# Performance work log

Measured on AMD Instinct MI355X. Metric: run time of the kernel, lower is better.

The kernel has to match this reference:

```python
import jax, jax.numpy as jnp
import numpy as np

EPS = 1e-5  # torch BatchNorm default eps


def _bn(x, g, b, axes):
    # Training-mode batch norm (biased variance, as torch uses for normalization)
    m = x.mean(axes, keepdims=True)
    v = x.var(axes, keepdims=True)
    sh = [1] * x.ndim
    sh[1] = x.shape[1]
    return (x - m) / jnp.sqrt(v + EPS) * g.reshape(sh) + b.reshape(sh)


def _conv2d(x, w, b, pad):
    y = jax.lax.conv_general_dilated(x, w, (1, 1), ((pad, pad), (pad, pad)),
                                     dimension_numbers=('NCHW', 'OIHW', 'NCHW'))
    return y + b.reshape(1, -1, 1, 1)


def _conv3d(x, w, b):
    # kernel (1,1,3), padding (0,0,1)
    y = jax.lax.conv_general_dilated(x, w, (1, 1, 1), ((0, 0), (0, 0), (1, 1)),
                                     dimension_numbers=('NCDHW', 'OIDHW', 'NCDHW'))
    return y + b.reshape(1, -1, 1, 1, 1)


def _block(x, w, b, g, be):
    return jax.nn.relu(_bn(_conv2d(x, w, b, 1), g, be, (0, 2, 3)))


def _pool(x):
    return jax.lax.reduce_window(x, -jnp.inf, jax.lax.max, (1, 1, 2, 2), (1, 1, 2, 2), 'VALID')


def _interp_axis(x, axis):
    # bilinear, align_corners=True, scale factor 2 along one axis
    n = x.shape[axis]
    out = 2 * n
    pos = jnp.linspace(0.0, n - 1.0, out)
    lo = jnp.floor(pos).astype(jnp.int32)
    hi = jnp.minimum(lo + 1, n - 1)
    w = (pos - lo).astype(x.dtype)
    sh = [1] * x.ndim
    sh[axis] = out
    w = w.reshape(sh)
    return jnp.take(x, lo, axis=axis) * (1 - w) + jnp.take(x, hi, axis=axis) * w


def _upsample(x):
    return _interp_axis(_interp_axis(x, 2), 3)


def _forward(x, tp_w1, tp_b1, tp_g1, tp_be1, tp_w2, tp_b2, tp_g2, tp_be2,
             range_w, doppler_w,
             enc1_w, enc1_b, enc1_g, enc1_be,
             enc2_w, enc2_b, enc2_g, enc2_be,
             enc3_w, enc3_b, enc3_g, enc3_be,
             dec3_w, dec3_b, dec3_g, dec3_be,
             dec2_w, dec2_b, dec2_g, dec2_be,
             dec1_w, dec1_b, dec1_g, dec1_be,
             out_w, out_b):
    # x: [B, RX, C, S, 2] -> [B, 2, RX, C, S]
    h = jnp.transpose(x, (0, 4, 1, 2, 3))
    h = jax.nn.relu(_bn(_conv3d(h, tp_w1, tp_b1), tp_g1, tp_be1, (0, 2, 3, 4)))
    h = jax.nn.relu(_bn(_conv3d(h, tp_w2, tp_b2), tp_g2, tp_be2, (0, 2, 3, 4)))
    h = jnp.transpose(h, (0, 2, 3, 4, 1)).sum(axis=1)  # sum over RX -> [B, C, S, 2]
    xr, xi = h[..., 0], h[..., 1]
    # Range DFT (quadruple loop in torch == two complex matmuls)
    Wr, Wi = range_w[..., 0], range_w[..., 1]  # [S, R]
    rr = jnp.einsum('bcs,sr->bcr', xr, Wr) - jnp.einsum('bcs,sr->bcr', xi, Wi)
    ri = jnp.einsum('bcs,sr->bcr', xr, Wi) + jnp.einsum('bcs,sr->bcr', xi, Wr)
    # Doppler DFT over chirps
    Dr, Di = doppler_w[..., 0], doppler_w[..., 1]  # [C, D]
    rdr = jnp.einsum('bcr,cd->bdr', rr, Dr) - jnp.einsum('bcr,cd->bdr', ri, Di)
    rdi = jnp.einsum('bcr,cd->bdr', rr, Di) + jnp.einsum('bcr,cd->bdr', ri, Dr)
    rd = jnp.stack([rdr, rdi], axis=1)  # [B, 2, D, R]
    # RadarNet U-Net
    e1 = _block(rd, enc1_w, enc1_b, enc1_g, enc1_be)
    p1 = _pool(e1)
    e2 = _block(p1, enc2_w, enc2_b, enc2_g, enc2_be)
    p2 = _pool(e2)
    e3 = _block(p2, enc3_w, enc3_b, enc3_g, enc3_be)
    d3 = _block(e3, dec3_w, dec3_b, dec3_g, dec3_be)
    u2 = _upsample(d3) + e2
    d2 = _block(u2, dec2_w, dec2_b, dec2_g, dec2_be)
    u1 = _upsample(d2) + e1
    d1 = _block(u1, dec1_w, dec1_b, dec1_g, dec1_be)
    out = jax.nn.sigmoid(_conv2d(d1, out_w, out_b, 0))
    return jnp.transpose(out, (0, 2, 3, 1))  # [B, D, R, 1]


def setup_inputs() -> dict:
    key = jax.random.key(0)
    ctr = [0]

    def rn(shape, scale=1.0):
        ctr[0] += 1
        return jax.random.normal(jax.random.fold_in(key, ctr[0]), shape, dtype=jnp.float32) * scale

    B, RX, C, S, D, R = 16, 4, 128, 256, 128, 256
    inp = {
        'x': rn((B, RX, C, S, 2)),
        'tp_w1': rn((8, 2, 1, 1, 3), 0.4), 'tp_b1': jnp.zeros(8), 'tp_g1': jnp.ones(8), 'tp_be1': jnp.zeros(8),
        'tp_w2': rn((2, 8, 1, 1, 3), 0.2), 'tp_b2': jnp.zeros(2), 'tp_g2': jnp.ones(2), 'tp_be2': jnp.zeros(2),
        'range_w': rn((S, R, 2)), 'doppler_w': rn((C, D, 2)),
        'enc1_w': rn((32, 2, 3, 3), 0.1), 'enc1_b': jnp.zeros(32), 'enc1_g': jnp.ones(32), 'enc1_be': jnp.zeros(32),
        'enc2_w': rn((64, 32, 3, 3), 0.05), 'enc2_b': jnp.zeros(64), 'enc2_g': jnp.ones(64), 'enc2_be': jnp.zeros(64),
        'enc3_w': rn((128, 64, 3, 3), 0.04), 'enc3_b': jnp.zeros(128), 'enc3_g': jnp.ones(128), 'enc3_be': jnp.zeros(128),
        'dec3_w': rn((64, 128, 3, 3), 0.03), 'dec3_b': jnp.zeros(64), 'dec3_g': jnp.ones(64), 'dec3_be': jnp.zeros(64),
        'dec2_w': rn((32, 64, 3, 3), 0.04), 'dec2_b': jnp.zeros(32), 'dec2_g': jnp.ones(32), 'dec2_be': jnp.zeros(32),
        'dec1_w': rn((16, 32, 3, 3), 0.05), 'dec1_b': jnp.zeros(16), 'dec1_g': jnp.ones(16), 'dec1_be': jnp.zeros(16),
        'out_w': rn((1, 16, 1, 1), 0.25), 'out_b': jnp.zeros(1),
    }
    return inp


def reference(x, tp_w1, tp_b1, tp_g1, tp_be1, tp_w2, tp_b2, tp_g2, tp_be2,
              range_w, doppler_w,
              enc1_w, enc1_b, enc1_g, enc1_be,
              enc2_w, enc2_b, enc2_g, enc2_be,
              enc3_w, enc3_b, enc3_g, enc3_be,
              dec3_w, dec3_b, dec3_g, dec3_be,
              dec2_w, dec2_b, dec2_g, dec2_be,
              dec1_w, dec1_b, dec1_g, dec1_be,
              out_w, out_b):
    return _forward(x, tp_w1, tp_b1, tp_g1, tp_be1, tp_w2, tp_b2, tp_g2, tp_be2,
                    range_w, doppler_w,
                    enc1_w, enc1_b, enc1_g, enc1_be,
                    enc2_w, enc2_b, enc2_g, enc2_be,
                    enc3_w, enc3_b, enc3_g, enc3_be,
                    dec3_w, dec3_b, dec3_g, dec3_be,
                    dec2_w, dec2_b, dec2_g, dec2_be,
                    dec1_w, dec1_b, dec1_g, dec1_be,
                    out_w, out_b)
```

## Files before the change

kernel.cpp:

```cpp
#include <hip/hip_runtime.h>
#include <cmath>

constexpr int Bn = 16, RXn = 4, Cn = 128, Sn = 256, Dn = 128, Rn = 256;

typedef __attribute__((ext_vector_type(8))) short bf16x8;
typedef __attribute__((ext_vector_type(4))) float f32x4;
typedef unsigned short u16;
typedef unsigned int u32;
typedef __attribute__((ext_vector_type(4))) u16 u16x4;
typedef __attribute__((ext_vector_type(8))) u16 u16x8;
typedef __attribute__((ext_vector_type(2))) u32 u32x2;
typedef __attribute__((ext_vector_type(4))) u32 u32x4;

__device__ __forceinline__ u16 f2bf(float f) {
  union { float f; u32 u; } v; v.f = f;
  const u32 r = v.u + 0x7FFFu + ((v.u >> 16) & 1u);
  return (u16)(r >> 16);
}
__device__ __forceinline__ float bf2f(u16 h) {
  union { u32 u; float f; } v; v.u = (u32)h << 16; return v.f;
}
__device__ __forceinline__ u32 cvtpk(float lo, float hi) {
  u32 r;
  asm("v_cvt_pk_bf16_f32 %0, %1, %2" : "=v"(r) : "v"(lo), "v"(hi));
  return r;
}
__device__ __forceinline__ void split2(float a, float b, u32& hi, u32& lo) {
  hi = cvtpk(a, b);
  union { u32 u; float f; } va, vb;
  va.u = hi << 16;
  vb.u = hi & 0xFFFF0000u;
  lo = cvtpk(a - va.f, b - vb.f);
}
__device__ __forceinline__ void ld8bf(const u16* __restrict__ p, float* v) {
  const u16x8 h = *(const u16x8*)p;
#pragma unroll
  for (int k = 0; k < 8; ++k) v[k] = bf2f(h[k]);
}

__device__ __forceinline__ void pack_seg(const float* __restrict__ w, u16* __restrict__ wpk,
                                         int CIN, int COUT, int gid, int gsz) {
  const int total = COUT * CIN * 9;
  const int chunks = CIN >> 5;
  for (int idx = gid; idx < total; idx += gsz) {
    const int j = idx & 7;
    const int l = (idx >> 3) & 63;
    const int rest = idx >> 9;
    const int t = rest % 9;
    const int rest2 = rest / 9;
    const int q = rest2 % chunks;
    const int mf = rest2 / chunks;
    const int co = mf * 16 + (l & 15);
    const int ci = q * 32 + ((l >> 4) << 3) + j;
    wpk[idx] = f2bf(w[((size_t)co * CIN + ci) * 9 + t]);
  }
}

__global__ __launch_bounds__(256) void k_pack_stats(
    const float* __restrict__ e2w, const float* __restrict__ e3w,
    const float* __restrict__ d3w, const float* __restrict__ d2w,
    const float* __restrict__ d1w,
    const float* __restrict__ range_w, const float* __restrict__ dopp_w,
    u16* __restrict__ p_e2, u16* __restrict__ p_e3,
    u16* __restrict__ p_d3, u16* __restrict__ p_d2,
    u16* __restrict__ p_d1,
    u16* __restrict__ A1h, u16* __restrict__ A1l,
    u16* __restrict__ A2h, u16* __restrict__ A2l,
    const float* __restrict__ x, const float* __restrict__ w1,
    float* __restrict__ part) {
  if (blockIdx.x < 128) {
    const int gid = blockIdx.x * 256 + threadIdx.x;
    const int gsz = 128 * 256;
    pack_seg(e2w, p_e2, 32, 64, gid, gsz);
    pack_seg(e3w, p_e3, 64, 128, gid, gsz);
    pack_seg(d3w, p_d3, 128, 64, gid, gsz);
    pack_seg(d2w, p_d2, 64, 32, gid, gsz);
    pack_seg(d1w, p_d1, 32, 16, gid, gsz);
    for (int idx = gid; idx < 512 * 512; idx += gsz) {
      const int m = idx >> 9, k = idx & 511;
      const int r = m >> 1, p = m & 1, s = k >> 1, q = k & 1;
      const float Wr = range_w[((size_t)s * Rn + r) * 2 + 0];
      const float Wi = range_w[((size_t)s * Rn + r) * 2 + 1];
      const float v = (p == 0) ? ((q == 0) ? Wr : -Wi) : ((q == 0) ? Wi : Wr);
      const u16 h = f2bf(v);
      A1h[idx] = h;
      A1l[idx] = f2bf(v - bf2f(h));
    }
    for (int idx = gid; idx < 256 * 256; idx += gsz) {
      const int m = idx >> 8, k = idx & 255;
      const int d = m >> 1, p = m & 1, c = k >> 1, q = k & 1;
      const float Dr = dopp_w[((size_t)c * Dn + d) * 2 + 0];
      const float Di = dopp_w[((size_t)c * Dn + d) * 2 + 1];
      const float v = (p == 0) ? ((q == 0) ? Dr : -Di) : ((q == 0) ? Di : Dr);
      const u16 h = f2bf(v);
      A2h[idx] = h;
      A2l[idx] = f2bf(v - bf2f(h));
    }
    return;
  }
  const int bx = blockIdx.x - 128;
  __shared__ float w1s[48];
  __shared__ float red8[8][4][2];
  const int t = threadIdx.x;
  if (t < 48) w1s[t] = w1[t];
  __syncthreads();
  float s1[8], s2[8];
#pragma unroll
  for (int o = 0; o < 8; ++o) { s1[o] = 0.f; s2[o] = 0.f; }
  for (int row = bx; row < Bn * RXn * Cn; row += 1024) {
    const float* xr = x + (size_t)row * Sn * 2;
    const float2 cc = *(const float2*)&xr[2 * t];
    const float2 mm = (t > 0) ? *(const float2*)&xr[2 * t - 2] : make_float2(0.f, 0.f);
    const float2 pp = (t < Sn - 1) ? *(const float2*)&xr[2 * t + 2] : make_float2(0.f, 0.f);
#pragma unroll
    for (int o = 0; o < 8; ++o) {
      const float* w = &w1s[o * 6];
      float h = w[0] * mm.x + w[1] * cc.x + w[2] * pp.x + w[3] * mm.y + w[4] * cc.y + w[5] * pp.y;
      s1[o] += h; s2[o] += h * h;
    }
  }
  const int lane = t & 63, wv = t >> 6;
#pragma unroll
  for (int o = 0; o < 8; ++o) {
    float v1 = s1[o], v2 = s2[o];
#pragma unroll
    for (int off = 32; off; off >>= 1) { v1 += __shfl_down(v1, off); v2 += __shfl_down(v2, off); }
    if (lane == 0) { red8[o][wv][0] = v1; red8[o][wv][1] = v2; }
  }
  __syncthreads();
  if (t < 8) {
    const float a1 = red8[t][0][0] + red8[t][1][0] + red8[t][2][0] + red8[t][3][0];
    const float a2 = red8[t][0][1] + red8[t][1][1] + red8[t][2][1] + red8[t][3][1];
    part[((size_t)t * 1024 + bx) * 2 + 0] = a1;
    part[((size_t)t * 1024 + bx) * 2 + 1] = a2;
  }
}

__global__ __launch_bounds__(256) void k_finalize(const float* __restrict__ part, int npart,
                                                  float n, const float* __restrict__ g,
                                                  const float* __restrict__ be,
                                                  float* __restrict__ stats) {
  const int co = blockIdx.x, t = threadIdx.x;
  __shared__ float r1[256], r2[256];
  float s1 = 0.f, s2 = 0.f;
  for (int i = t; i < npart; i += 256) {
    s1 += part[((size_t)co * npart + i) * 2 + 0];
    s2 += part[((size_t)co * npart + i) * 2 + 1];
  }
  r1[t] = s1; r2[t] = s2;
  __syncthreads();
  for (int off = 128; off; off >>= 1) {
    if (t < off) { r1[t] += r1[t + off]; r2[t] += r2[t + off]; }
    __syncthreads();
  }
  if (t == 0) {
    const float mean = r1[0] / n;
    const float var  = fmaxf(r2[0] / n - mean * mean, 0.f);
    const float inv  = rsqrtf(var + 1e-5f);
    const float sc   = inv * g[co];
    stats[2 * co + 0] = sc;
    stats[2 * co + 1] = be[co] - mean * sc;
  }
}

__global__ __launch_bounds__(256) void k_tp_fused2(const float* __restrict__ x,
                                                   const float* __restrict__ w1,
                                                   const float* __restrict__ st1,
                                                   const float* __restrict__ w2,
                                                   u32* __restrict__ h2p,
                                                   float* __restrict__ part) {
  __shared__ float a1[8][Sn + 2];
  __shared__ float w1s[48], w2s[48], st[16];
  __shared__ float red2s[2][4][2];
  const int t = threadIdx.x;
  const int row = blockIdx.x;
  if (t < 48) { w1s[t] = w1[t]; w2s[t] = w2[t]; }
  if (t < 16) st[t] = st1[t];
  __syncthreads();
  const float* xr = x + (size_t)row * Sn * 2;
  const float2 cc = *(const float2*)&xr[2 * t];
  const float2 mm = (t > 0) ? *(const float2*)&xr[2 * t - 2] : make_float2(0.f, 0.f);
  const float2 pp = (t < Sn - 1) ? *(const float2*)&xr[2 * t + 2] : make_float2(0.f, 0.f);
#pragma unroll
  for (int o = 0; o < 8; ++o) {
    const float* w = &w1s[o * 6];
    float h = w[0] * mm.x + w[1] * cc.x + w[2] * pp.x + w[3] * mm.y + w[4] * cc.y + w[5] * pp.y;
    float v = fmaf(h, st[2 * o], st[2 * o + 1]);
    a1[o][1 + t] = v > 0.f ? v : 0.f;
    if (t == 0) { a1[o][0] = 0.f; a1[o][Sn + 1] = 0.f; }
  }
  __syncthreads();
  float h2v[2];
#pragma unroll
  for (int j = 0; j < 2; ++j) {
    float acc = 0.f;
#pragma unroll
    for (int o = 0; o < 8; ++o) {
      const float* w = &w2s[j * 24 + o * 3];
      acc += w[0] * a1[o][t] + w[1] * a1[o][t + 1] + w[2] * a1[o][t + 2];
    }
    h2v[j] = acc;
  }
  h2p[(size_t)row * Sn + t] = cvtpk(h2v[0], h2v[1]);
  const int lane = t & 63, wv = t >> 6;
#pragma unroll
  for (int j = 0; j < 2; ++j) {
    float v1 = h2v[j], v2 = h2v[j] * h2v[j];
#pragma unroll
    for (int off = 32; off; off >>= 1) { v1 += __shfl_down(v1, off); v2 += __shfl_down(v2, off); }
    if (lane == 0) { red2s[j][wv][0] = v1; red2s[j][wv][1] = v2; }
  }
  __syncthreads();
  if (t < 2) {
    const float a1s = red2s[t][0][0] + red2s[t][1][0] + red2s[t][2][0] + red2s[t][3][0];
    const float a2s = red2s[t][0][1] + red2s[t][1][1] + red2s[t][2][1] + red2s[t][3][1];
    part[((size_t)t * gridDim.x + row) * 2 + 0] = a1s;
    part[((size_t)t * gridDim.x + row) * 2 + 1] = a2s;
  }
}

__global__ __launch_bounds__(256) void k_prep(const u32* __restrict__ h2p,
                                              const float* __restrict__ st2,
                                              u32* __restrict__ B1h32,
                                              u32* __restrict__ B1l32) {
  const int row = blockIdx.x;
  const int s = threadIdx.x;
  const int b = row >> 7, c = row & (Cn - 1);
  const float sc0 = st2[0], sh0 = st2[1], sc1 = st2[2], sh1 = st2[3];
  float xr = 0.f, xi = 0.f;
#pragma unroll
  for (int rx = 0; rx < RXn; ++rx) {
    const u32 v = h2p[(((size_t)b * RXn + rx) * Cn + c) * Sn + s];
    const float vr = bf2f((u16)(v & 0xFFFFu));
    const float vi = bf2f((u16)(v >> 16));
    xr += fmaxf(fmaf(vr, sc0, sh0), 0.f);
    xi += fmaxf(fmaf(vi, sc1, sh1), 0.f);
  }
  u32 hi, lo;
  split2(xr, xi, hi, lo);
  B1h32[(size_t)row * 256 + s] = hi;
  B1l32[(size_t)row * 256 + s] = lo;
}

template <int M, int N, int K, int STORE>
__global__ __launch_bounds__(256) void k_gemm_split(const u16* __restrict__ Ah,
                                                    const u16* __restrict__ Al,
                                                    const u16* __restrict__ Bh,
                                                    const u16* __restrict__ Bl,
                                                    u32* __restrict__ out0,
                                                    u32* __restrict__ out1) {
  __shared__ __align__(16) u16 lah[32 * 40], lal[32 * 40];
  __shared__ __align__(16) u16 lbh[64 * 40], lbl[64 * 40];
  const int tid = threadIdx.x;
  const int lane = tid & 63, wid = tid >> 6;
  const int wm = wid >> 1, wn = wid & 1;
  const int l15 = lane & 15, lg = lane >> 4;
  const int m0 = blockIdx.x * 32, n0 = blockIdx.y * 64;
  f32x4 acc[2];
  acc[0] = (f32x4){0.f, 0.f, 0.f, 0.f};
  acc[1] = (f32x4){0.f, 0.f, 0.f, 0.f};
  const int arow = tid >> 3, ak = (tid & 7) * 4;
  const int brow = tid >> 2, bk = (tid & 3) * 8;
  for (int k0 = 0; k0 < K; k0 += 32) {
    *(u16x4*)&lah[arow * 40 + ak] = *(const u16x4*)&Ah[(size_t)(m0 + arow) * K + k0 + ak];
    *(u16x4*)&lal[arow * 40 + ak] = *(const u16x4*)&Al[(size_t)(m0 + arow) * K + k0 + ak];
    *(u16x8*)&lbh[brow * 40 + bk] = *(const u16x8*)&Bh[(size_t)(n0 + brow) * K + k0 + bk];
    *(u16x8*)&lbl[brow * 40 + bk] = *(const u16x8*)&Bl[(size_t)(n0 + brow) * K + k0 + bk];
    __syncthreads();
    const bf16x8 ah = *(const bf16x8*)&lah[(wm * 16 + l15) * 40 + lg * 8];
    const bf16x8 al = *(const bf16x8*)&lal[(wm * 16 + l15) * 40 + lg * 8];
#pragma unroll
    for (int f = 0; f < 2; ++f) {
      const bf16x8 bh = *(const bf16x8*)&lbh[(wn * 32 + f * 16 + l15) * 40 + lg * 8];
      const bf16x8 bl = *(const bf16x8*)&lbl[(wn * 32 + f * 16 + l15) * 40 + lg * 8];
      acc[f] = __builtin_amdgcn_mfma_f32_16x16x32_bf16(ah, bh, acc[f], 0, 0, 0);
      acc[f] = __builtin_amdgcn_mfma_f32_16x16x32_bf16(ah, bl, acc[f], 0, 0, 0);
      acc[f] = __builtin_amdgcn_mfma_f32_16x16x32_bf16(al, bh, acc[f], 0, 0, 0);
    }
    __syncthreads();
  }
  const int mb = m0 + wm * 16 + lg * 4;
#pragma unroll
  for (int f = 0; f < 2; ++f) {
    const int n = n0 + wn * 32 + f * 16 + l15;
    if (STORE == 0) {
      const int b = n >> 7, c = n & 127;
#pragma unroll
      for (int pair = 0; pair < 2; ++pair) {
        const int r = (mb >> 1) + pair;
        u32 hi, lo;
        split2(acc[f][2 * pair], acc[f][2 * pair + 1], hi, lo);
        const size_t idx = ((size_t)b * 256 + r) * 128 + c;
        out0[idx] = hi;
        out1[idx] = lo;
      }
    } else {
      const int b = n >> 8, r = n & 255;
#pragma unroll
      for (int pair = 0; pair < 2; ++pair) {
        const int d = (mb >> 1) + pair;
        out0[((size_t)b * 128 + d) * 256 + r] = cvtpk(acc[f][2 * pair], acc[f][2 * pair + 1]);
      }
    }
  }
}

template <int CIN, int COUT, int H, int W, int TH, int TW, int MW, int NW,
          int WAVES_M, int WAVES_N, int MODE>
__global__ __launch_bounds__(256) void k_conv_mfma(const u16* __restrict__ in,
                                                   const u16* __restrict__ wpk,
                                                   const float* __restrict__ in_stats,
                                                   const u16* __restrict__ in2,
                                                   const float* __restrict__ in2_stats,
                                                   u16* __restrict__ out,
                                                   float* __restrict__ part) {
  constexpr int COG = WAVES_M * MW * 16;
  constexpr int CHUNKS = CIN / 32;
  constexpr int NFROW = TW / 16;
  constexpr int XROWS = TH + 2, XCOLS = TW + 2;
  static_assert(WAVES_M * WAVES_N == 4, "waves");
  static_assert(WAVES_N * NW * 16 == TH * TW, "pixel cover");
  __shared__ __align__(16) u16 xs[XROWS * XCOLS * 40];
  __shared__ float red1[WAVES_N][COG], red2[WAVES_N][COG];
  __shared__ __align__(16) float sst1[2 * CIN];
  __shared__ __align__(16) float sst2[(MODE == 3) ? 2 * CIN : 4];
  const int tid = threadIdx.x;
  const int lane = tid & 63;
  const int wid = tid >> 6;
  const int wave_m = wid / WAVES_N;
  const int wave_n = wid % WAVES_N;
  const int l15 = lane & 15, lg = lane >> 4;
  constexpr int TILES_W = W / TW;
  const int tile = blockIdx.x;
  const int tw = tile % TILES_W, th = tile / TILES_W;
  const int h0 = th * TH, w0 = tw * TW;
  const int cog = blockIdx.y, b = blockIdx.z;
  for (int i = tid; i < 2 * CIN; i += 256) sst1[i] = in_stats[i];
  if (MODE == 3)
    for (int i = tid; i < 2 * CIN; i += 256) sst2[i] = in2_stats[i];
  __syncthreads();
  f32x4 acc[MW][NW];
#pragma unroll
  for (int m = 0; m < MW; ++m)
#pragma unroll
    for (int f = 0; f < NW; ++f) acc[m][f] = (f32x4){0.f, 0.f, 0.f, 0.f};

  for (int q = 0; q < CHUNKS; ++q) {
    const int ci0 = (tid & 3) * 8;
    const int cch = q * 32 + ci0;
    float sc[8], sh[8];
#pragma unroll
    for (int k = 0; k < 4; ++k) {
      const float4 qq = *(const float4*)&sst1[2 * cch + 4 * k];
      sc[2 * k] = qq.x; sh[2 * k] = qq.y; sc[2 * k + 1] = qq.z; sh[2 * k + 1] = qq.w;
    }
    float ec[8], es[8];
    if constexpr (MODE == 3) {
#pragma unroll
      for (int k = 0; k < 4; ++k) {
        const float4 qq = *(const float4*)&sst2[2 * cch + 4 * k];
        ec[2 * k] = qq.x; es[2 * k] = qq.y; ec[2 * k + 1] = qq.z; es[2 * k + 1] = qq.w;
      }
    }
    for (int i = tid; i < XROWS * XCOLS * 4; i += 256) {
      const int pix = i >> 2;
      const int col = pix % XCOLS;
      const int row = pix / XCOLS;
      const int gh = h0 + row - 1, gw = w0 + col - 1;
      u32x4 enc = (u32x4){0u, 0u, 0u, 0u};
      if (gh >= 0 && gh < H && gw >= 0 && gw < W) {
        float vv[8];
        if constexpr (MODE == 1) {
          float tv[8];
          ld8bf(&in[(((size_t)b * H + gh) * W + gw) * CIN + cch], tv);
#pragma unroll
          for (int k = 0; k < 8; ++k) vv[k] = fmaxf(fmaf(tv[k], sc[k], sh[k]), 0.f);
        } else if constexpr (MODE == 2) {
          const size_t rs = (size_t)(2 * W) * CIN;
          const u16* pb = &in[(((size_t)b * 2 * H + 2 * gh) * (2 * W) + 2 * gw) * CIN + cch];
          float tp[4][8];
          ld8bf(pb, tp[0]);
          ld8bf(pb + CIN, tp[1]);
          ld8bf(pb + rs, tp[2]);
          ld8bf(pb + rs + CIN, tp[3]);
#pragma unroll
          for (int k = 0; k < 8; ++k) {
            const float mx = fmaxf(fmaxf(tp[0][k], tp[1][k]), fmaxf(tp[2][k], tp[3][k]));
            vv[k] = fmaxf(fmaf(mx, sc[k], sh[k]), 0.f);
          }
        } else {
          constexpr int Hi2 = H / 2, Wi2 = W / 2;
          constexpr float steph = (float)(Hi2 - 1) / (float)(H - 1);
          constexpr float stepw = (float)(Wi2 - 1) / (float)(W - 1);
          const float ph = (float)gh * steph;
          const int hlo = (int)ph;
          const int hhi = (hlo + 1 < Hi2) ? hlo + 1 : Hi2 - 1;
          const float fh = ph - (float)hlo;
          const float pw = (float)gw * stepw;
          const int wl = (int)pw;
          const int wh = (wl + 1 < Wi2) ? wl + 1 : Wi2 - 1;
          const float fw = pw - (float)wl;
          const float w00 = (1.f - fh) * (1.f - fw), w01 = (1.f - fh) * fw;
          const float w10 = fh * (1.f - fw), w11 = fh * fw;
          const u16* dbase = &in[(size_t)b * Hi2 * Wi2 * CIN + cch];
          float tp[4][8];
          ld8bf(dbase + ((size_t)hlo * Wi2 + wl) * CIN, tp[0]);
          ld8bf(dbase + ((size_t)hlo * Wi2 + wh) * CIN, tp[1]);
          ld8bf(dbase + ((size_t)hhi * Wi2 + wl) * CIN, tp[2]);
          ld8bf(dbase + ((size_t)hhi * Wi2 + wh) * CIN, tp[3]);
          float ev[8];
          ld8bf(&in2[(((size_t)b * H + gh) * W + gw) * CIN + cch], ev);
#pragma unroll
          for (int k = 0; k < 8; ++k) {
            const float a = fmaxf(fmaf(tp[0][k], sc[k], sh[k]), 0.f);
            const float bb = fmaxf(fmaf(tp[1][k], sc[k], sh[k]), 0.f);
            const float cc = fmaxf(fmaf(tp[2][k], sc[k], sh[k]), 0.f);
            const float dd = fmaxf(fmaf(tp[3][k], sc[k], sh[k]), 0.f);
            vv[k] = w00 * a + w01 * bb + w10 * cc + w11 * dd
                  + fmaxf(fmaf(ev[k], ec[k], es[k]), 0.f);
          }
        }
#pragma unroll
        for (int j = 0; j < 4; ++j) enc[j] = cvtpk(vv[2 * j], vv[2 * j + 1]);
      }
      *(u32x4*)&xs[(row * XCOLS + col) * 40 + ci0] = enc;
    }
    __syncthreads();
#pragma unroll
    for (int t = 0; t < 9; ++t) {
      const int ky = t / 3, kx = t % 3;
      bf16x8 afr[MW];
#pragma unroll
      for (int m = 0; m < MW; ++m) {
        const int mfg = cog * (COG / 16) + wave_m * MW + m;
        afr[m] = *(const bf16x8*)&wpk[((((size_t)mfg * CHUNKS + q) * 9 + t) * 64 + lane) * 8];
      }
      bf16x8 bfr[NW];
#pragma unroll
      for (int f = 0; f < NW; ++f) {
        const int nf = wave_n * NW + f;
        const int r = nf / NFROW;
        const int cseg = (nf % NFROW) * 16;
        bfr[f] = *(const bf16x8*)&xs[((r + ky) * XCOLS + (cseg + l15 + kx)) * 40 + lg * 8];
      }
#pragma unroll
      for (int m = 0; m < MW; ++m)
#pragma unroll
        for (int f = 0; f < NW; ++f)
          acc[m][f] = __builtin_amdgcn_mfma_f32_16x16x32_bf16(afr[m], bfr[f], acc[m][f], 0, 0, 0);
    }
    __syncthreads();
  }

#pragma unroll
  for (int m = 0; m < MW; ++m) {
    const int cobase = cog * COG + (wave_m * MW + m) * 16 + lg * 4;
#pragma unroll
    for (int f = 0; f < NW; ++f) {
      const int nf = wave_n * NW + f;
      const int r = nf / NFROW;
      const int cseg = (nf % NFROW) * 16;
      u16* op = out + (((size_t)b * H + h0 + r) * W + (w0 + cseg + l15)) * COUT + cobase;
      u32x2 ov;
      ov[0] = cvtpk(acc[m][f][0], acc[m][f][1]);
      ov[1] = cvtpk(acc[m][f][2], acc[m][f][3]);
      *(u32x2*)op = ov;
    }
  }
#pragma unroll
  for (int m = 0; m < MW; ++m)
#pragma unroll
    for (int reg = 0; reg < 4; ++reg) {
      float s1 = 0.f, s2 = 0.f;
#pragma unroll
      for (int f = 0; f < NW; ++f) { const float v = acc[m][f][reg]; s1 += v; s2 += v * v; }
#pragma unroll
      for (int off = 1; off < 16; off <<= 1) { s1 += __shfl_xor(s1, off); s2 += __shfl_xor(s2, off); }
      if (l15 == 0) {
        const int ch = (wave_m * MW + m) * 16 + lg * 4 + reg;
        red1[wave_n][ch] = s1; red2[wave_n][ch] = s2;
      }
    }
  __syncthreads();
  if (tid < COG) {
    float s1 = 0.f, s2 = 0.f;
#pragma unroll
    for (int wn = 0; wn < WAVES_N; ++wn) { s1 += red1[wn][tid]; s2 += red2[wn][tid]; }
    const int npart = gridDim.x * gridDim.z;
    const int pidx = blockIdx.z * gridDim.x + blockIdx.x;
    part[((size_t)(cog * COG + tid) * npart + pidx) * 2 + 0] = s1;
    part[((size_t)(cog * COG + tid) * npart + pidx) * 2 + 1] = s2;
  }
}

__global__ __launch_bounds__(256) void k_conv1(const u32* __restrict__ in,
                                               const float* __restrict__ wgt,
                                               u16* __restrict__ out,
                                               float* __restrict__ part) {
  constexpr int H = 128, W = 256, TW = 64, TH = 16, COG = 16, COUT = 32;
  const int tid = threadIdx.x;
  const int tile = blockIdx.x;
  const int tw = tile & 3, th = tile >> 2;
  const int cog = blockIdx.y, b = blockIdx.z;
  const int ty = tid >> 4;
  const int wofs = (tid & 15) * 4;
  const int h0 = th * TH, w0t = tw * TW;
  __shared__ float xs0[TH + 2][TW + 3], xs1[TH + 2][TW + 3];
  __shared__ float ws[2][COG][12];
  __shared__ float redp[4][COG], redq[4][COG];
  for (int i = tid; i < 2 * COG * 9; i += 256) {
    const int tap = i % 9, rest = i / 9;
    const int ci = rest & 1, co = rest >> 1;
    ws[ci][co][tap] = wgt[((size_t)(cog * COG + co) * 2 + ci) * 9 + tap];
  }
  for (int i = tid; i < (TH + 2) * (TW + 2); i += 256) {
    const int col = i % (TW + 2), row = i / (TW + 2);
    const int gh = h0 + row - 1, gw = w0t + col - 1;
    float v0 = 0.f, v1 = 0.f;
    if (gh >= 0 && gh < H && gw >= 0 && gw < W) {
      const u32 v = in[((size_t)b * H + gh) * W + gw];
      v0 = bf2f((u16)(v & 0xFFFFu));
      v1 = bf2f((u16)(v >> 16));
    }
    xs0[row][col] = v0; xs1[row][col] = v1;
  }
  __syncthreads();
  float acc[4][COG];
#pragma unroll
  for (int px = 0; px < 4; ++px)
#pragma unroll
    for (int co = 0; co < COG; ++co) acc[px][co] = 0.f;
#pragma unroll
  for (int ci = 0; ci < 2; ++ci) {
    float xrow[3][6];
#pragma unroll
    for (int ky = 0; ky < 3; ++ky)
#pragma unroll
      for (int j = 0; j < 6; ++j)
        xrow[ky][j] = ci ? xs1[ty + ky][wofs + j] : xs0[ty + ky][wofs + j];
#pragma unroll
    for (int co = 0; co < COG; ++co) {
      const float4 wq0 = *(const float4*)&ws[ci][co][0];
      const float4 wq1 = *(const float4*)&ws[ci][co][4];
      const float  w8 = ws[ci][co][8];
      const float wv[9] = {wq0.x, wq0.y, wq0.z, wq0.w, wq1.x, wq1.y, wq1.z, wq1.w, w8};
#pragma unroll
      for (int ky = 0; ky < 3; ++ky)
#pragma unroll
        for (int kx = 0; kx < 3; ++kx)
#pragma unroll
          for (int px = 0; px < 4; ++px)
            acc[px][co] = fmaf(xrow[ky][px + kx], wv[ky * 3 + kx], acc[px][co]);
    }
  }
#pragma unroll
  for (int px = 0; px < 4; ++px) {
    u16* op = out + (((size_t)b * H + h0 + ty) * W + (w0t + wofs + px)) * COUT + cog * COG;
    u32x4 ov;
    ov[0] = cvtpk(acc[px][0], acc[px][1]);
    ov[1] = cvtpk(acc[px][2], acc[px][3]);
    ov[2] = cvtpk(acc[px][4], acc[px][5]);
    ov[3] = cvtpk(acc[px][6], acc[px][7]);
    *(u32x4*)&op[0] = ov;
    u32x4 ov2;
    ov2[0] = cvtpk(acc[px][8], acc[px][9]);
    ov2[1] = cvtpk(acc[px][10], acc[px][11]);
    ov2[2] = cvtpk(acc[px][12], acc[px][13]);
    ov2[3] = cvtpk(acc[px][14], acc[px][15]);
    *(u32x4*)&op[8] = ov2;
  }
  const int lane = tid & 63, wid = tid >> 6;
#pragma unroll
  for (int co = 0; co < COG; ++co) {
    float v1 = 0.f, v2 = 0.f;
#pragma unroll
    for (int px = 0; px < 4; ++px) { v1 += acc[px][co]; v2 += acc[px][co] * acc[px][co]; }
#pragma unroll
    for (int off = 32; off; off >>= 1) { v1 += __shfl_down(v1, off); v2 += __shfl_down(v2, off); }
    if (lane == 0) { redp[wid][co] = v1; redq[wid][co] = v2; }
  }
  __syncthreads();
  if (tid < COG) {
    const int npart = gridDim.x * gridDim.z;
    const int pidx = blockIdx.z * gridDim.x + blockIdx.x;
    part[((size_t)(cog * COG + tid) * npart + pidx) * 2 + 0] = redp[0][tid] + redp[1][tid] + redp[2][tid] + redp[3][tid];
    part[((size_t)(cog * COG + tid) * npart + pidx) * 2 + 1] = redq[0][tid] + redq[1][tid] + redq[2][tid] + redq[3][tid];
  }
}

__global__ __launch_bounds__(256) void k_out_bn(const u16* __restrict__ d1,
                                                const float* __restrict__ st,
                                                const float* __restrict__ ow,
                                                const float* __restrict__ ob,
                                                float* __restrict__ out) {
  const size_t i = (size_t)blockIdx.x * 256 + threadIdx.x;
  const size_t total = (size_t)Bn * Dn * Rn;
  if (i >= total) return;
  const u16* p = d1 + i * 16;
  float v[16];
  ld8bf(p, v);
  ld8bf(p + 8, v + 8);
  float acc = ob[0];
#pragma unroll
  for (int k = 0; k < 16; ++k) {
    const float2 q = *(const float2*)&st[2 * k];
    acc += fmaxf(fmaf(v[k], q.x, q.y), 0.f) * ow[k];
  }
  out[i] = 1.f / (1.f + expf(-acc));
}

extern "C" void kernel_launch(void* const* d_in, const int* in_sizes, int n_in,
                              void* d_out, int out_size, void* d_ws, size_t ws_size,
                              hipStream_t stream) {
  (void)in_sizes; (void)n_in; (void)out_size; (void)ws_size;
  const float* x       = (const float*)d_in[0];
  const float* tp_w1   = (const float*)d_in[1];
  const float* tp_g1   = (const float*)d_in[3];
  const float* tp_be1  = (const float*)d_in[4];
  const float* tp_w2   = (const float*)d_in[5];
  const float* tp_g2   = (const float*)d_in[7];
  const float* tp_be2  = (const float*)d_in[8];
  const float* range_w = (const float*)d_in[9];
  const float* dopp_w  = (const float*)d_in[10];
  const float* e1w = (const float*)d_in[11]; const float* e1g = (const float*)d_in[13]; const float* e1b = (const float*)d_in[14];
  const float* e2w = (const float*)d_in[15]; const float* e2g = (const float*)d_in[17]; const float* e2b = (const float*)d_in[18];
  const float* e3w = (const float*)d_in[19]; const float* e3g = (const float*)d_in[21]; const float* e3b = (const float*)d_in[22];
  const float* d3w = (const float*)d_in[23]; const float* d3g = (const float*)d_in[25]; const float* d3b = (const float*)d_in[26];
  const float* d2w = (const float*)d_in[27]; const float* d2g = (const float*)d_in[29]; const float* d2b = (const float*)d_in[30];
  const float* d1w = (const float*)d_in[31]; const float* d1g = (const float*)d_in[33]; const float* d1b = (const float*)d_in[34];
  const float* out_w = (const float*)d_in[35];
  const float* out_b = (const float*)d_in[36];
  float* outp = (float*)d_out;

  float* W  = (float*)d_ws;
  u16* Ae1  = (u16*)W;
  float* Bx = W + 16777216;
  u16* Ce2  = (u16*)(W + 33554432);
  u16* Ee3  = (u16*)(W + 41943040);
  u16* Fd3  = (u16*)(W + 46137344);
  float* part  = W + 48234496;
  float* stats = part + 262144;
  u16* wpk_e2 = (u16*)(stats + 1024);
  u16* wpk_e3 = wpk_e2 + 18432;
  u16* wpk_d3 = wpk_e3 + 73728;
  u16* wpk_d2 = wpk_d3 + 73728;
  u16* wpk_d1 = wpk_d2 + 18432;
  u16* A1h = wpk_d1 + 4608;
  u16* A1l = A1h + 262144;
  u16* A2h = A1l + 262144;
  u16* A2l = A2h + 65536;
  u16* B1h = A2l + 65536;
  u16* B1l = B1h + 1048576;
  u16* B2h = B1l + 1048576;
  u16* B2l = B2h + 1048576;

  u32* h2p = (u32*)Bx;
  u32* rd  = (u32*)(Bx + 2097152 + 65536);
  u16* d1  = (u16*)Bx;

  float* st_tp1 = stats;
  float* st_tp2 = stats + 16;
  float* st_e1  = stats + 32;
  float* st_e2  = stats + 96;
  float* st_e3  = stats + 224;
  float* st_d3  = stats + 480;
  float* st_d2  = stats + 608;
  float* st_d1  = stats + 672;

  const float Ntp = 2097152.f;

  k_pack_stats<<<1152, 256, 0, stream>>>(e2w, e3w, d3w, d2w, d1w, range_w, dopp_w,
                                         wpk_e2, wpk_e3, wpk_d3, wpk_d2, wpk_d1,
                                         A1h, A1l, A2h, A2l,
                                         x, tp_w1, part);
  k_finalize<<<8, 256, 0, stream>>>(part, 1024, Ntp, tp_g1, tp_be1, st_tp1);
  k_tp_fused2<<<Bn * RXn * Cn, 256, 0, stream>>>(x, tp_w1, st_tp1, tp_w2, h2p, part);
  k_finalize<<<2, 256, 0, stream>>>(part, Bn * RXn * Cn, Ntp, tp_g2, tp_be2, st_tp2);

  k_prep<<<Bn * Cn, 256, 0, stream>>>(h2p, st_tp2, (u32*)B1h, (u32*)B1l);
  k_gemm_split<512, 2048, 512, 0><<<dim3(16, 32), 256, 0, stream>>>(
      A1h, A1l, B1h, B1l, (u32*)B2h, (u32*)B2l);
  k_gemm_split<256, 4096, 256, 1><<<dim3(8, 64), 256, 0, stream>>>(
      A2h, A2l, B2h, B2l, rd, nullptr);

  k_conv1<<<dim3(32, 2, Bn), 256, 0, stream>>>(rd, e1w, Ae1, part);
  k_finalize<<<32, 256, 0, stream>>>(part, 512, 524288.f, e1g, e1b, st_e1);
  k_conv_mfma<32, 64, 64, 128, 8, 32, 2, 8, 2, 2, 2><<<dim3(32, 1, Bn), 256, 0, stream>>>(
      Ae1, wpk_e2, st_e1, nullptr, nullptr, Ce2, part);
  k_finalize<<<64, 256, 0, stream>>>(part, 512, 131072.f, e2g, e2b, st_e2);
  k_conv_mfma<64, 128, 32, 64, 4, 16, 1, 4, 4, 1, 2><<<dim3(32, 2, Bn), 256, 0, stream>>>(
      Ce2, wpk_e3, st_e2, nullptr, nullptr, Ee3, part);
  k_finalize<<<128, 256, 0, stream>>>(part, 512, 32768.f, e3g, e3b, st_e3);
  k_conv_mfma<128, 64, 32, 64, 4, 16, 1, 4, 4, 1, 1><<<dim3(32, 1, Bn), 256, 0, stream>>>(
      Ee3, wpk_d3, st_e3, nullptr, nullptr, Fd3, part);
  k_finalize<<<64, 256, 0, stream>>>(part, 512, 32768.f, d3g, d3b, st_d3);
  k_conv_mfma<64, 32, 64, 128, 8, 32, 1, 8, 2, 2, 3><<<dim3(32, 1, Bn), 256, 0, stream>>>(
      Fd3, wpk_d2, st_d3, Ce2, st_e2, Ee3, part);
  k_finalize<<<32, 256, 0, stream>>>(part, 512, 131072.f, d2g, d2b, st_d2);
  k_conv_mfma<32, 16, 128, 256, 8, 32, 1, 4, 1, 4, 3><<<dim3(128, 1, Bn), 256, 0, stream>>>(
      Ee3, wpk_d1, st_d2, Ae1, st_e1, d1, part);
  k_finalize<<<16, 256, 0, stream>>>(part, 2048, 524288.f, d1g, d1b, st_d1);
  k_out_bn<<<2048, 256, 0, stream>>>(d1, st_d1, out_w, out_b, outp);
}
```

Before: 222.9 us.

## Split upsample+skip-add out of decoder convs into separate elementwise kernel

Moves the bilinear upsample, BN-ReLU and skip-add for the two decoder convolutions out of the conv halo-loading loop into a standalone elementwise kernel that writes a materialised bf16 tensor. The convs then load that tensor directly (new MODE 0) with no per-element math. This removes the redundant recomputation of the halo and the 5-way gather inside the conv tile loop. In exchange it adds two kernel launches and an extra full-resolution write and read through global memory.

```diff
diff --git a/kernel.cpp b/kernel.cpp
--- a/kernel.cpp
+++ b/kernel.cpp
@@ -305,13 +305,71 @@
   }
 }
 
+template <int C, int H, int W>
+__global__ __launch_bounds__(256) void k_upsum(const u16* __restrict__ din,
+                                               const float* __restrict__ dst,
+                                               const u16* __restrict__ skip,
+                                               const float* __restrict__ kst,
+                                               u16* __restrict__ outp) {
+  constexpr int C8 = C / 8;
+  const int idx = blockIdx.x * 256 + threadIdx.x;
+  const int total = Bn * H * W * C8;
+  if (idx >= total) return;
+  const int c8 = idx % C8;
+  const int w = (idx / C8) % W;
+  const int h = (idx / (C8 * W)) % H;
+  const int b = idx / (C8 * W * H);
+  const int c0 = c8 * 8;
+  float sc[8], sh[8], ec[8], es[8];
+#pragma unroll
+  for (int k = 0; k < 4; ++k) {
+    const float4 q1 = *(const float4*)&dst[2 * c0 + 4 * k];
+    sc[2 * k] = q1.x; sh[2 * k] = q1.y; sc[2 * k + 1] = q1.z; sh[2 * k + 1] = q1.w;
+    const float4 q2 = *(const float4*)&kst[2 * c0 + 4 * k];
+    ec[2 * k] = q2.x; es[2 * k] = q2.y; ec[2 * k + 1] = q2.z; es[2 * k + 1] = q2.w;
+  }
+  constexpr int Hi2 = H / 2, Wi2 = W / 2;
+  constexpr float steph = (float)(Hi2 - 1) / (float)(H - 1);
+  constexpr float stepw = (float)(Wi2 - 1) / (float)(W - 1);
+  const float ph = (float)h * steph;
+  const int hlo = (int)ph;
+  const int hhi = (hlo + 1 < Hi2) ? hlo + 1 : Hi2 - 1;
+  const float fh = ph - (float)hlo;
+  const float pw = (float)w * stepw;
+  const int wl = (int)pw;
+  const int wh = (wl + 1 < Wi2) ? wl + 1 : Wi2 - 1;
+  const float fw = pw - (float)wl;
+  const float w00 = (1.f - fh) * (1.f - fw), w01 = (1.f - fh) * fw;
+  const float w10 = fh * (1.f - fw), w11 = fh * fw;
+  const u16* dbase = &din[(size_t)b * Hi2 * Wi2 * C + c0];
+  float tp[4][8];
+  ld8bf(dbase + ((size_t)hlo * Wi2 + wl) * C, tp[0]);
+  ld8bf(dbase + ((size_t)hlo * Wi2 + wh) * C, tp[1]);
+  ld8bf(dbase + ((size_t)hhi * Wi2 + wl) * C, tp[2]);
+  ld8bf(dbase + ((size_t)hhi * Wi2 + wh) * C, tp[3]);
+  float ev[8];
+  ld8bf(&skip[(((size_t)b * H + h) * W + w) * C + c0], ev);
+  float vv[8];
+#pragma unroll
+  for (int k = 0; k < 8; ++k) {
+    const float a  = fmaxf(fmaf(tp[0][k], sc[k], sh[k]), 0.f);
+    const float bb = fmaxf(fmaf(tp[1][k], sc[k], sh[k]), 0.f);
+    const float cc = fmaxf(fmaf(tp[2][k], sc[k], sh[k]), 0.f);
+    const float dd = fmaxf(fmaf(tp[3][k], sc[k], sh[k]), 0.f);
+    vv[k] = w00 * a + w01 * bb + w10 * cc + w11 * dd
+          + fmaxf(fmaf(ev[k], ec[k], es[k]), 0.f);
+  }
+  u32x4 enc;
+#pragma unroll
+  for (int j = 0; j < 4; ++j) enc[j] = cvtpk(vv[2 * j], vv[2 * j + 1]);
+  *(u32x4*)&outp[(((size_t)b * H + h) * W + w) * C + c0] = enc;
+}
+
 template <int CIN, int COUT, int H, int W, int TH, int TW, int MW, int NW,
           int WAVES_M, int WAVES_N, int MODE>
 __global__ __launch_bounds__(256) void k_conv_mfma(const u16* __restrict__ in,
                                                    const u16* __restrict__ wpk,
                                                    const float* __restrict__ in_stats,
-                                                   const u16* __restrict__ in2,
-                                                   const float* __restrict__ in2_stats,
                                                    u16* __restrict__ out,
                                                    float* __restrict__ part) {
   constexpr int COG = WAVES_M * MW * 16;
@@ -322,8 +380,7 @@
   static_assert(WAVES_N * NW * 16 == TH * TW, "pixel cover");
   __shared__ __align__(16) u16 xs[XROWS * XCOLS * 40];
   __shared__ float red1[WAVES_N][COG], red2[WAVES_N][COG];
-  __shared__ __align__(16) float sst1[2 * CIN];
-  __shared__ __align__(16) float sst2[(MODE == 3) ? 2 * CIN : 4];
+  __shared__ __align__(16) float sst1[(MODE == 0) ? 4 : 2 * CIN];
   const int tid = threadIdx.x;
   const int lane = tid & 63;
   const int wid = tid >> 6;
@@ -335,9 +392,9 @@
   const int tw = tile % TILES_W, th = tile / TILES_W;
   const int h0 = th * TH, w0 = tw * TW;
   const int cog = blockIdx.y, b = blockIdx.z;
-  for (int i = tid; i < 2 * CIN; i += 256) sst1[i] = in_stats[i];
-  if (MODE == 3)
-    for (int i = tid; i < 2 * CIN; i += 256) sst2[i] = in2_stats[i];
+  if constexpr (MODE != 0) {
+    for (int i = tid; i < 2 * CIN; i += 256) sst1[i] = in_stats[i];
+  }
   __syncthreads();
   f32x4 acc[MW][NW];
 #pragma unroll
@@ -349,17 +406,11 @@
     const int ci0 = (tid & 3) * 8;
     const int cch = q * 32 + ci0;
     float sc[8], sh[8];
-#pragma unroll
-    for (int k = 0; k < 4; ++k) {
-      const float4 qq = *(const float4*)&sst1[2 * cch + 4 * k];
-      sc[2 * k] = qq.x; sh[2 * k] = qq.y; sc[2 * k + 1] = qq.z; sh[2 * k + 1] = qq.w;
-    }
-    float ec[8], es[8];
-    if constexpr (MODE == 3) {
+    if constexpr (MODE != 0) {
 #pragma unroll
       for (int k = 0; k < 4; ++k) {
-        const float4 qq = *(const float4*)&sst2[2 * cch + 4 * k];
-        ec[2 * k] = qq.x; es[2 * k] = qq.y; ec[2 * k + 1] = qq.z; es[2 * k + 1] = qq.w;
+        const float4 qq = *(const float4*)&sst1[2 * cch + 4 * k];
+        sc[2 * k] = qq.x; sh[2 * k] = qq.y; sc[2 * k + 1] = qq.z; sh[2 * k + 1] = qq.w;
       }
     }
     for (int i = tid; i < XROWS * XCOLS * 4; i += 256) {
@@ -369,13 +420,18 @@
       const int gh = h0 + row - 1, gw = w0 + col - 1;
       u32x4 enc = (u32x4){0u, 0u, 0u, 0u};
       if (gh >= 0 && gh < H && gw >= 0 && gw < W) {
-        float vv[8];
-        if constexpr (MODE == 1) {
+        if constexpr (MODE == 0) {
+          enc = *(const u32x4*)&in[(((size_t)b * H + gh) * W + gw) * CIN + cch];
+        } else if constexpr (MODE == 1) {
+          float vv[8];
           float tv[8];
           ld8bf(&in[(((size_t)b * H + gh) * W + gw) * CIN + cch], tv);
 #pragma unroll
           for (int k = 0; k < 8; ++k) vv[k] = fmaxf(fmaf(tv[k], sc[k], sh[k]), 0.f);
-        } else if constexpr (MODE == 2) {
+#pragma unroll
+          for (int j = 0; j < 4; ++j) enc[j] = cvtpk(vv[2 * j], vv[2 * j + 1]);
+        } else {
+          float vv[8];
           const size_t rs = (size_t)(2 * W) * CIN;
           const u16* pb = &in[(((size_t)b * 2 * H + 2 * gh) * (2 * W) + 2 * gw) * CIN + cch];
           float tp[4][8];
@@ -388,40 +444,9 @@
             const float mx = fmaxf(fmaxf(tp[0][k], tp[1][k]), fmaxf(tp[2][k], tp[3][k]));
             vv[k] = fmaxf(fmaf(mx, sc[k], sh[k]), 0.f);
           }
-        } else {
-          constexpr int Hi2 = H / 2, Wi2 = W / 2;
-          constexpr float steph = (float)(Hi2 - 1) / (float)(H - 1);
-          constexpr float stepw = (float)(Wi2 - 1) / (float)(W - 1);
-          const float ph = (float)gh * steph;
-          const int hlo = (int)ph;
-          const int hhi = (hlo + 1 < Hi2) ? hlo + 1 : Hi2 - 1;
-          const float fh = ph - (float)hlo;
-          const float pw = (float)gw * stepw;
-          const int wl = (int)pw;
-          const int wh = (wl + 1 < Wi2) ? wl + 1 : Wi2 - 1;
-          const float fw = pw - (float)wl;
-          const float w00 = (1.f - fh) * (1.f - fw), w01 = (1.f - fh) * fw;
-          const float w10 = fh * (1.f - fw), w11 = fh * fw;
-          const u16* dbase = &in[(size_t)b * Hi2 * Wi2 * CIN + cch];
-          float tp[4][8];
-          ld8bf(dbase + ((size_t)hlo * Wi2 + wl) * CIN, tp[0]);
-          ld8bf(dbase + ((size_t)hlo * Wi2 + wh) * CIN, tp[1]);
-          ld8bf(dbase + ((size_t)hhi * Wi2 + wl) * CIN, tp[2]);
-          ld8bf(dbase + ((size_t)hhi * Wi2 + wh) * CIN, tp[3]);
-          float ev[8];
-          ld8bf(&in2[(((size_t)b * H + gh) * W + gw) * CIN + cch], ev);
-#pragma unroll
-          for (int k = 0; k < 8; ++k) {
-            const float a = fmaxf(fmaf(tp[0][k], sc[k], sh[k]), 0.f);
-            const float bb = fmaxf(fmaf(tp[1][k], sc[k], sh[k]), 0.f);
-            const float cc = fmaxf(fmaf(tp[2][k], sc[k], sh[k]), 0.f);
-            const float dd = fmaxf(fmaf(tp[3][k], sc[k], sh[k]), 0.f);
-            vv[k] = w00 * a + w01 * bb + w10 * cc + w11 * dd
-                  + fmaxf(fmaf(ev[k], ec[k], es[k]), 0.f);
-          }
+#pragma unroll
+          for (int j = 0; j < 4; ++j) enc[j] = cvtpk(vv[2 * j], vv[2 * j + 1]);
         }
-#pragma unroll
-        for (int j = 0; j < 4; ++j) enc[j] = cvtpk(vv[2 * j], vv[2 * j + 1]);
       }
       *(u32x4*)&xs[(row * XCOLS + col) * 40 + ci0] = enc;
     }
@@ -657,6 +682,8 @@
   u32* h2p = (u32*)Bx;
   u32* rd  = (u32*)(Bx + 2097152 + 65536);
   u16* d1  = (u16*)Bx;
+  u16* U2  = (u16*)(Bx + 4194304);
+  u16* U1  = (u16*)(Bx + 8388608);
 
   float* st_tp1 = stats;
   float* st_tp2 = stats + 16;
@@ -686,19 +713,21 @@
   k_conv1<<<dim3(32, 2, Bn), 256, 0, stream>>>(rd, e1w, Ae1, part);
   k_finalize<<<32, 256, 0, stream>>>(part, 512, 524288.f, e1g, e1b, st_e1);
   k_conv_mfma<32, 64, 64, 128, 8, 32, 2, 8, 2, 2, 2><<<dim3(32, 1, Bn), 256, 0, stream>>>(
-      Ae1, wpk_e2, st_e1, nullptr, nullptr, Ce2, part);
+      Ae1, wpk_e2, st_e1, Ce2, part);
   k_finalize<<<64, 256, 0, stream>>>(part, 512, 131072.f, e2g, e2b, st_e2);
   k_conv_mfma<64, 128, 32, 64, 4, 16, 1, 4, 4, 1, 2><<<dim3(32, 2, Bn), 256, 0, stream>>>(
-      Ce2, wpk_e3, st_e2, nullptr, nullptr, Ee3, part);
+      Ce2, wpk_e3, st_e2, Ee3, part);
   k_finalize<<<128, 256, 0, stream>>>(part, 512, 32768.f, e3g, e3b, st_e3);
   k_conv_mfma<128, 64, 32, 64, 4, 16, 1, 4, 4, 1, 1><<<dim3(32, 1, Bn), 256, 0, stream>>>(
-      Ee3, wpk_d3, st_e3, nullptr, nullptr, Fd3, part);
+      Ee3, wpk_d3, st_e3, Fd3, part);
   k_finalize<<<64, 256, 0, stream>>>(part, 512, 32768.f, d3g, d3b, st_d3);
-  k_conv_mfma<64, 32, 64, 128, 8, 32, 1, 8, 2, 2, 3><<<dim3(32, 1, Bn), 256, 0, stream>>>(
-      Fd3, wpk_d2, st_d3, Ce2, st_e2, Ee3, part);
+  k_upsum<64, 64, 128><<<4096, 256, 0, stream>>>(Fd3, st_d3, Ce2, st_e2, U2);
+  k_conv_mfma<64, 32, 64, 128, 8, 32, 1, 8, 2, 2, 0><<<dim3(32, 1, Bn), 256, 0, stream>>>(
+      U2, wpk_d2, nullptr, Ee3, part);
   k_finalize<<<32, 256, 0, stream>>>(part, 512, 131072.f, d2g, d2b, st_d2);
-  k_conv_mfma<32, 16, 128, 256, 8, 32, 1, 4, 1, 4, 3><<<dim3(128, 1, Bn), 256, 0, stream>>>(
-      Ee3, wpk_d1, st_d2, Ae1, st_e1, d1, part);
+  k_upsum<32, 128, 256><<<8192, 256, 0, stream>>>(Ee3, st_d2, Ae1, st_e1, U1);
+  k_conv_mfma<32, 16, 128, 256, 8, 32, 1, 4, 1, 4, 0><<<dim3(128, 1, Bn), 256, 0, stream>>>(
+      U1, wpk_d1, nullptr, d1, part);
   k_finalize<<<16, 256, 0, stream>>>(part, 2048, 524288.f, d1g, d1b, st_d1);
   k_out_bn<<<2048, 256, 0, stream>>>(d1, st_d1, out_w, out_b, outp);
 }
```

After: 240.6 us. 1.08x slower.
